# Performance work log

Measured on AMD Instinct MI355X. Metric: run time of the kernel, lower is better.

Reference implementation:

```python
import jax, jax.numpy as jnp
import numpy as np

B, N = 4, 128
INPUT_SIZE, Z_SIZE = 512, 256
D_TENSOR, N_HEADS, SEQ_LEN = 64, 8, 64
D = D_TENSOR * N_HEADS * SEQ_LEN  # 32768


def setup_inputs() -> dict:
    key = jax.random.key(0)
    ks = jax.random.split(key, 10)
    s = lambda fan_in: 1.0 / np.sqrt(fan_in)
    return {
        "x": jax.random.normal(ks[0], (B, N, INPUT_SIZE), dtype=jnp.float32),
        "z": jax.random.normal(ks[1], (B, N, Z_SIZE), dtype=jnp.float32),
        "Wq": jax.random.uniform(ks[2], (Z_SIZE, D), jnp.float32, -s(Z_SIZE), s(Z_SIZE)),
        "bq": jax.random.uniform(ks[3], (D,), jnp.float32, -s(Z_SIZE), s(Z_SIZE)),
        "Wk": jax.random.uniform(ks[4], (INPUT_SIZE, D), jnp.float32, -s(INPUT_SIZE), s(INPUT_SIZE)),
        "bk": jax.random.uniform(ks[5], (D,), jnp.float32, -s(INPUT_SIZE), s(INPUT_SIZE)),
        "Wv": jax.random.uniform(ks[6], (INPUT_SIZE, D), jnp.float32, -s(INPUT_SIZE), s(INPUT_SIZE)),
        "bv": jax.random.uniform(ks[7], (D,), jnp.float32, -s(INPUT_SIZE), s(INPUT_SIZE)),
        "Wo": jax.random.uniform(ks[8], (D, INPUT_SIZE), jnp.float32, -s(D), s(D)),
        "bo": jax.random.uniform(ks[9], (INPUT_SIZE,), jnp.float32, -s(D), s(D)),
    }


def reference(x, z, Wq, bq, Wk, bk, Wv, bv, Wo, bo):
    # Q, K, V: [B, N, heads, seq_len, d_tensor]
    Q = (z @ Wq + bq).reshape(B, N, N_HEADS, SEQ_LEN, D_TENSOR)
    K = (x @ Wk + bk).reshape(B, N, N_HEADS, SEQ_LEN, D_TENSOR)
    V = (x @ Wv + bv).reshape(B, N, N_HEADS, SEQ_LEN, D_TENSOR)
    scores = jnp.einsum("bnhqd,bnhkd->bnhqk", Q, K) / np.sqrt(D_TENSOR).astype(np.float32)
    attn = jax.nn.softmax(scores, axis=-1)
    out = jnp.einsum("bnhqk,bnhkd->bnhqd", attn, V).reshape(B, N, D)
    return out @ Wo + bo
```

## Files before the change

### kernel.cpp

```cpp
#include <hip/hip_runtime.h>
#include <stdint.h>


typedef __attribute__((ext_vector_type(8))) short short8;
typedef __attribute__((ext_vector_type(4))) float floatx4;

__device__ __forceinline__ unsigned short f2bf(float f) {
  union { float f; unsigned int u; } v; v.f = f;
  unsigned int u = v.u + 0x7FFFu + ((v.u >> 16) & 1u);
  return (unsigned short)(u >> 16);
}

#define MFMA16(a, b, c) __builtin_amdgcn_mfma_f32_16x16x32_bf16((a), (b), (c), 0, 0, 0)

#define STAGE_TILE(SRC, LD, LDSARR)                                            \
  do {                                                                         \
    _Pragma("unroll") for (int i_ = 0; i_ < 4; ++i_) {                         \
      int e_ = tid + (i_ << 8);                                                \
      int r_ = e_ >> 3;                                                        \
      int c_ = (e_ & 7) ^ (r_ & 7);                                            \
      __builtin_amdgcn_global_load_lds(                                        \
          (const __attribute__((address_space(1))) unsigned int*)((SRC) +      \
              (size_t)r_ * (LD) + (c_ << 3)),                                  \
          (__attribute__((address_space(3))) unsigned int*)(&(LDSARR)[e_ << 3]),\
          16, 0, 0);                                                           \
    }                                                                          \
  } while (0)

#define FRAG(LDSARR, ROW, KS)                                                  \
  (*(const short8*)(&(LDSARR)[(((ROW) << 6)) +                                 \
      ((((((KS) << 2) + quad)) ^ ((ROW) & 7)) << 3)]))

__device__ __forceinline__ void transpose_body(const float* __restrict__ W,
                                               unsigned short* __restrict__ WT,
                                               int Kd, int Nd) {
  __shared__ __align__(16) float S[64 * 72];
  __shared__ __align__(16) unsigned short T[64 * 72];
  const int tid = threadIdx.x;
  const int n0 = blockIdx.x * 64, k0 = blockIdx.y * 64;
#pragma unroll
  for (int i = 0; i < 4; ++i) {
    int e = tid + (i << 8);
    int r = e >> 4, c = (e & 15) << 2;
    float4 w = *(const float4*)(W + (size_t)(k0 + r) * Nd + n0 + c);
    *(float4*)(&S[r * 72 + c]) = w;
  }
  __syncthreads();
  {
    const int n = tid & 63, kh = tid >> 6;
    float v[16];
#pragma unroll
    for (int j = 0; j < 16; ++j) v[j] = S[(kh * 16 + j) * 72 + n];
    uint4 p0, p1;
    p0.x = f2bf(v[0])  | ((unsigned)f2bf(v[1])  << 16);
    p0.y = f2bf(v[2])  | ((unsigned)f2bf(v[3])  << 16);
    p0.z = f2bf(v[4])  | ((unsigned)f2bf(v[5])  << 16);
    p0.w = f2bf(v[6])  | ((unsigned)f2bf(v[7])  << 16);
    p1.x = f2bf(v[8])  | ((unsigned)f2bf(v[9])  << 16);
    p1.y = f2bf(v[10]) | ((unsigned)f2bf(v[11]) << 16);
    p1.z = f2bf(v[12]) | ((unsigned)f2bf(v[13]) << 16);
    p1.w = f2bf(v[14]) | ((unsigned)f2bf(v[15]) << 16);
    *(uint4*)(&T[n * 72 + kh * 16])     = p0;
    *(uint4*)(&T[n * 72 + kh * 16 + 8]) = p1;
  }
  __syncthreads();
#pragma unroll
  for (int i = 0; i < 2; ++i) {
    int e = tid + (i << 8);
    int n = e >> 3, kc = e & 7;
    uint4 vv = *(const uint4*)(&T[n * 72 + kc * 8]);
    *(uint4*)(WT + (size_t)(n0 + n) * Kd + k0 + kc * 8) = vv;
  }
}

__global__ __launch_bounds__(256) void transpose_qkv(const float* __restrict__ Wq,
                                                     const float* __restrict__ Wk,
                                                     const float* __restrict__ Wv,
                                                     unsigned short* __restrict__ WqT,
                                                     unsigned short* __restrict__ WkT,
                                                     unsigned short* __restrict__ WvT,
                                                     const float* __restrict__ x,
                                                     const float* __restrict__ z,
                                                     unsigned short* __restrict__ xb,
                                                     unsigned short* __restrict__ zb) {
  const int zsel = blockIdx.z;
  if (zsel == 0) {
    if (blockIdx.y >= 4) return;
    transpose_body(Wq, WqT, 256, 32768);
  } else if (zsel == 1) {
    transpose_body(Wk, WkT, 512, 32768);
  } else if (zsel == 2) {
    transpose_body(Wv, WvT, 512, 32768);
  } else {
    if (blockIdx.y != 0 || blockIdx.x >= 192) return;
    int idx = (blockIdx.x * 256 + threadIdx.x) * 8;
    const float* src;
    unsigned short* dst;
    if (idx < 262144) { src = x + idx; dst = xb + idx; }
    else              { src = z + (idx - 262144); dst = zb + (idx - 262144); }
    float4 f0 = *(const float4*)src;
    float4 f1 = *(const float4*)(src + 4);
    uint4 p;
    p.x = f2bf(f0.x) | ((unsigned)f2bf(f0.y) << 16);
    p.y = f2bf(f0.z) | ((unsigned)f2bf(f0.w) << 16);
    p.z = f2bf(f1.x) | ((unsigned)f2bf(f1.y) << 16);
    p.w = f2bf(f1.z) | ((unsigned)f2bf(f1.w) << 16);
    *(uint4*)dst = p;
  }
}

__global__ __launch_bounds__(256) void transpose_wo(const float* __restrict__ W,
                                                    unsigned short* __restrict__ WT) {
  transpose_body(W, WT, 32768, 512);
}

__global__ __launch_bounds__(256) void gemm_qkv(const unsigned short* __restrict__ xb,
                                                const unsigned short* __restrict__ zb,
                                                const unsigned short* __restrict__ WqT,
                                                const unsigned short* __restrict__ WkT,
                                                const unsigned short* __restrict__ WvT,
                                                const float* __restrict__ bq,
                                                const float* __restrict__ bk,
                                                const float* __restrict__ bv,
                                                unsigned short* __restrict__ Qb,
                                                unsigned short* __restrict__ Kb,
                                                unsigned short* __restrict__ Vb) {
  __shared__ __align__(16) unsigned short As[128 * 64];
  __shared__ __align__(16) unsigned short Bs[128 * 64];
  const int tid = threadIdx.x;
  const int zsel = blockIdx.z;
  const unsigned short* A;
  const unsigned short* BT;
  const float* bias;
  unsigned short* C;
  int Ka;
  if (zsel == 0)      { A = zb; BT = WqT; bias = bq; C = Qb; Ka = 256; }
  else if (zsel == 1) { A = xb; BT = WkT; bias = bk; C = Kb; Ka = 512; }
  else                { A = xb; BT = WvT; bias = bv; C = Vb; Ka = 512; }
  const int lane = tid & 63, wid = tid >> 6;
  const int quad = lane >> 4, l15 = lane & 15;
  const int wm = wid >> 1, wn = wid & 1;
  const int m0 = blockIdx.y * 128, n0 = blockIdx.x * 128;
  floatx4 acc[4][4] = {};
  for (int k0 = 0; k0 < Ka; k0 += 64) {
    STAGE_TILE(A + (size_t)m0 * Ka + k0, Ka, As);
    STAGE_TILE(BT + (size_t)n0 * Ka + k0, Ka, Bs);
    __syncthreads();
#pragma unroll
    for (int ks = 0; ks < 2; ++ks) {
      short8 aF[4], bF[4];
#pragma unroll
      for (int mi = 0; mi < 4; ++mi) aF[mi] = FRAG(As, wm * 64 + mi * 16 + l15, ks);
#pragma unroll
      for (int ni = 0; ni < 4; ++ni) bF[ni] = FRAG(Bs, wn * 64 + ni * 16 + l15, ks);
#pragma unroll
      for (int mi = 0; mi < 4; ++mi)
#pragma unroll
        for (int ni = 0; ni < 4; ++ni)
          acc[mi][ni] = MFMA16(aF[mi], bF[ni], acc[mi][ni]);
    }
    __syncthreads();
  }
#pragma unroll
  for (int ni = 0; ni < 4; ++ni) {
    int col = n0 + wn * 64 + ni * 16 + l15;
    float bv2 = bias[col];
#pragma unroll
    for (int mi = 0; mi < 4; ++mi) {
      int row = m0 + wm * 64 + mi * 16 + (quad << 2);
#pragma unroll
      for (int r = 0; r < 4; ++r)
        C[(size_t)(row + r) * 32768 + col] = f2bf(acc[mi][ni][r] + bv2);
    }
  }
}

__global__ __launch_bounds__(256) void attn64(const unsigned short* __restrict__ Qb,
                                              const unsigned short* __restrict__ Kb,
                                              const unsigned short* __restrict__ Vb,
                                              unsigned short* __restrict__ Ob) {
  __shared__ __align__(16) unsigned short Qs[64 * 72];
  __shared__ __align__(16) unsigned short Ks[64 * 72];
  __shared__ __align__(16) unsigned short VT[64 * 72];
  __shared__ __align__(16) unsigned short Ps[64 * 72];
  const int tid = threadIdx.x;
  const int bn = blockIdx.x >> 3, h = blockIdx.x & 7;
  const size_t base = (size_t)bn * 32768 + (size_t)h * 4096;
  const unsigned short* q = Qb + base;
  const unsigned short* k = Kb + base;
  const unsigned short* v = Vb + base;
#pragma unroll
  for (int i = 0; i < 2; ++i) {
    int e = tid + (i << 8);
    int r = e >> 3, dblk = e & 7;
    *(uint4*)(&Qs[r * 72 + dblk * 8]) = *(const uint4*)(q + r * 64 + dblk * 8);
    *(uint4*)(&Ks[r * 72 + dblk * 8]) = *(const uint4*)(k + r * 64 + dblk * 8);
    uint4 vv = *(const uint4*)(v + r * 64 + dblk * 8);
    const unsigned short* pv = (const unsigned short*)&vv;
#pragma unroll
    for (int j = 0; j < 8; ++j)
      VT[(dblk * 8 + j) * 72 + r] = pv[j];
  }
  __syncthreads();
  const int lane = tid & 63, wid = tid >> 6;
  const int quad = lane >> 4, l15 = lane & 15;
  const int qs = wid << 4;
  short8 aq0 = *(const short8*)(&Qs[(qs + l15) * 72 + quad * 8]);
  short8 aq1 = *(const short8*)(&Qs[(qs + l15) * 72 + 32 + quad * 8]);
  floatx4 s[4] = {};
#pragma unroll
  for (int ni = 0; ni < 4; ++ni) {
    short8 b0 = *(const short8*)(&Ks[(ni * 16 + l15) * 72 + quad * 8]);
    short8 b1 = *(const short8*)(&Ks[(ni * 16 + l15) * 72 + 32 + quad * 8]);
    s[ni] = MFMA16(aq0, b0, s[ni]);
    s[ni] = MFMA16(aq1, b1, s[ni]);
  }
#pragma unroll
  for (int r = 0; r < 4; ++r) {
    float e0 = s[0][r] * 0.125f, e1 = s[1][r] * 0.125f;
    float e2 = s[2][r] * 0.125f, e3 = s[3][r] * 0.125f;
    float m = fmaxf(fmaxf(e0, e1), fmaxf(e2, e3));
    m = fmaxf(m, __shfl_xor(m, 1));
    m = fmaxf(m, __shfl_xor(m, 2));
    m = fmaxf(m, __shfl_xor(m, 4));
    m = fmaxf(m, __shfl_xor(m, 8));
    float x0 = __expf(e0 - m), x1 = __expf(e1 - m);
    float x2 = __expf(e2 - m), x3 = __expf(e3 - m);
    float t = x0 + x1 + x2 + x3;
    t += __shfl_xor(t, 1); t += __shfl_xor(t, 2);
    t += __shfl_xor(t, 4); t += __shfl_xor(t, 8);
    float inv = __builtin_amdgcn_rcpf(t);
    int row = qs + (quad << 2) + r;
    Ps[row * 72 +      l15] = f2bf(x0 * inv);
    Ps[row * 72 + 16 + l15] = f2bf(x1 * inv);
    Ps[row * 72 + 32 + l15] = f2bf(x2 * inv);
    Ps[row * 72 + 48 + l15] = f2bf(x3 * inv);
  }
  __syncthreads();
  short8 ap0 = *(const short8*)(&Ps[(qs + l15) * 72 + quad * 8]);
  short8 ap1 = *(const short8*)(&Ps[(qs + l15) * 72 + 32 + quad * 8]);
  floatx4 o[4] = {};
#pragma unroll
  for (int ni = 0; ni < 4; ++ni) {
    short8 b0 = *(const short8*)(&VT[(ni * 16 + l15) * 72 + quad * 8]);
    short8 b1 = *(const short8*)(&VT[(ni * 16 + l15) * 72 + 32 + quad * 8]);
    o[ni] = MFMA16(ap0, b0, o[ni]);
    o[ni] = MFMA16(ap1, b1, o[ni]);
  }
  unsigned short* outp = Ob + base;
#pragma unroll
  for (int ni = 0; ni < 4; ++ni)
#pragma unroll
    for (int r = 0; r < 4; ++r)
      outp[(qs + (quad << 2) + r) * 64 + ni * 16 + l15] = f2bf(o[ni][r]);
}

__global__ __launch_bounds__(256) void gemm_out(const unsigned short* __restrict__ A,
                                                const unsigned short* __restrict__ BT,
                                                const float* __restrict__ bias,
                                                float* __restrict__ C) {
  __shared__ __align__(16) unsigned short As[128 * 64];
  __shared__ __align__(16) unsigned short Bs[128 * 64];
  const int tid = threadIdx.x;
  const int lane = tid & 63, wid = tid >> 6;
  const int quad = lane >> 4, l15 = lane & 15;
  const int wm = wid >> 1, wn = wid & 1;
  const int m0 = blockIdx.y * 128, n0 = blockIdx.x * 128;
  const int kbase = blockIdx.z * 1024;
  floatx4 acc[4][4] = {};
  for (int k0 = kbase; k0 < kbase + 1024; k0 += 64) {
    STAGE_TILE(A + (size_t)m0 * 32768 + k0, 32768, As);
    STAGE_TILE(BT + (size_t)n0 * 32768 + k0, 32768, Bs);
    __syncthreads();
#pragma unroll
    for (int ks = 0; ks < 2; ++ks) {
      short8 aF[4], bF[4];
#pragma unroll
      for (int mi = 0; mi < 4; ++mi) aF[mi] = FRAG(As, wm * 64 + mi * 16 + l15, ks);
#pragma unroll
      for (int ni = 0; ni < 4; ++ni) bF[ni] = FRAG(Bs, wn * 64 + ni * 16 + l15, ks);
#pragma unroll
      for (int mi = 0; mi < 4; ++mi)
#pragma unroll
        for (int ni = 0; ni < 4; ++ni)
          acc[mi][ni] = MFMA16(aF[mi], bF[ni], acc[mi][ni]);
    }
    __syncthreads();
  }
#pragma unroll
  for (int ni = 0; ni < 4; ++ni) {
    int col = n0 + wn * 64 + ni * 16 + l15;
    float bv = (blockIdx.z == 0) ? bias[col] : 0.0f;
#pragma unroll
    for (int mi = 0; mi < 4; ++mi) {
      int row = m0 + wm * 64 + mi * 16 + (quad << 2);
#pragma unroll
      for (int r = 0; r < 4; ++r)
        atomicAdd(&C[(size_t)(row + r) * 512 + col], acc[mi][ni][r] + bv);
    }
  }
}

extern "C" void kernel_launch(void* const* d_in, const int* in_sizes, int n_in,
                              void* d_out, int out_size, void* d_ws, size_t ws_size,
                              hipStream_t stream) {
  const float* x  = (const float*)d_in[0];
  const float* z  = (const float*)d_in[1];
  const float* Wq = (const float*)d_in[2];
  const float* bq = (const float*)d_in[3];
  const float* Wk = (const float*)d_in[4];
  const float* bk = (const float*)d_in[5];
  const float* Wv = (const float*)d_in[6];
  const float* bv = (const float*)d_in[7];
  const float* Wo = (const float*)d_in[8];
  const float* bo = (const float*)d_in[9];
  float* out = (float*)d_out;
  char* ws = (char*)d_ws;

  unsigned short* WqT = (unsigned short*)(ws + 0);
  unsigned short* WkT = (unsigned short*)(ws + 16777216);
  unsigned short* WvT = (unsigned short*)(ws + 50331648);
  unsigned short* Qb  = (unsigned short*)(ws + 83886080);
  unsigned short* Kb  = (unsigned short*)(ws + 117440512);
  unsigned short* Vb  = (unsigned short*)(ws + 150994944);
  unsigned short* Ob  = (unsigned short*)(ws + 0);
  unsigned short* WoT = (unsigned short*)(ws + 50331648);

  unsigned short* xb = (unsigned short*)d_out;
  unsigned short* zb = (unsigned short*)((char*)d_out + 524288);

  transpose_qkv<<<dim3(512, 8, 4), 256, 0, stream>>>(Wq, Wk, Wv, WqT, WkT, WvT,
                                                     x, z, xb, zb);

  gemm_qkv<<<dim3(256, 4, 3), 256, 0, stream>>>(xb, zb, WqT, WkT, WvT,
                                                bq, bk, bv, Qb, Kb, Vb);

  transpose_wo<<<dim3(8, 512), 256, 0, stream>>>(Wo, WoT);

  attn64<<<dim3(4096), 256, 0, stream>>>(Qb, Kb, Vb, Ob);

  hipMemsetAsync(d_out, 0, (size_t)out_size * sizeof(float), stream);
  gemm_out<<<dim3(4, 4, 32), 256, 0, stream>>>(Ob, WoT, bo, out);
}
```

Measured before the change: 384.7 us.

## Fuse fp32 weight conversion into GEMM B-tile staging and drop transpose kernels

```diff
diff --git a/kernel.cpp b/kernel.cpp
--- a/kernel.cpp
+++ b/kernel.cpp
@@ -9,6 +9,12 @@
   union { float f; unsigned int u; } v; v.f = f;
   unsigned int u = v.u + 0x7FFFu + ((v.u >> 16) & 1u);
   return (unsigned short)(u >> 16);
+}
+
+__device__ __forceinline__ unsigned int cvt_pk_bf16(float lo, float hi) {
+  unsigned int r;
+  asm("v_cvt_pk_bf16_f32 %0, %1, %2" : "=v"(r) : "v"(lo), "v"(hi));
+  return r;
 }
 
 #define MFMA16(a, b, c) __builtin_amdgcn_mfma_f32_16x16x32_bf16((a), (b), (c), 0, 0, 0)
@@ -31,120 +37,80 @@
   (*(const short8*)(&(LDSARR)[(((ROW) << 6)) +                                 \
       ((((((KS) << 2) + quad)) ^ ((ROW) & 7)) << 3)]))
 
-__device__ __forceinline__ void transpose_body(const float* __restrict__ W,
-                                               unsigned short* __restrict__ WT,
-                                               int Kd, int Nd) {
-  __shared__ __align__(16) float S[64 * 72];
-  __shared__ __align__(16) unsigned short T[64 * 72];
-  const int tid = threadIdx.x;
-  const int n0 = blockIdx.x * 64, k0 = blockIdx.y * 64;
-#pragma unroll
-  for (int i = 0; i < 4; ++i) {
-    int e = tid + (i << 8);
-    int r = e >> 4, c = (e & 15) << 2;
-    float4 w = *(const float4*)(W + (size_t)(k0 + r) * Nd + n0 + c);
-    *(float4*)(&S[r * 72 + c]) = w;
-  }
-  __syncthreads();
-  {
-    const int n = tid & 63, kh = tid >> 6;
-    float v[16];
-#pragma unroll
-    for (int j = 0; j < 16; ++j) v[j] = S[(kh * 16 + j) * 72 + n];
-    uint4 p0, p1;
-    p0.x = f2bf(v[0])  | ((unsigned)f2bf(v[1])  << 16);
-    p0.y = f2bf(v[2])  | ((unsigned)f2bf(v[3])  << 16);
-    p0.z = f2bf(v[4])  | ((unsigned)f2bf(v[5])  << 16);
-    p0.w = f2bf(v[6])  | ((unsigned)f2bf(v[7])  << 16);
-    p1.x = f2bf(v[8])  | ((unsigned)f2bf(v[9])  << 16);
-    p1.y = f2bf(v[10]) | ((unsigned)f2bf(v[11]) << 16);
-    p1.z = f2bf(v[12]) | ((unsigned)f2bf(v[13]) << 16);
-    p1.w = f2bf(v[14]) | ((unsigned)f2bf(v[15]) << 16);
-    *(uint4*)(&T[n * 72 + kh * 16])     = p0;
-    *(uint4*)(&T[n * 72 + kh * 16 + 8]) = p1;
-  }
-  __syncthreads();
-#pragma unroll
-  for (int i = 0; i < 2; ++i) {
-    int e = tid + (i << 8);
-    int n = e >> 3, kc = e & 7;
-    uint4 vv = *(const uint4*)(&T[n * 72 + kc * 8]);
-    *(uint4*)(WT + (size_t)(n0 + n) * Kd + k0 + kc * 8) = vv;
-  }
-}
-
-__global__ __launch_bounds__(256) void transpose_qkv(const float* __restrict__ Wq,
-                                                     const float* __restrict__ Wk,
-                                                     const float* __restrict__ Wv,
-                                                     unsigned short* __restrict__ WqT,
-                                                     unsigned short* __restrict__ WkT,
-                                                     unsigned short* __restrict__ WvT,
-                                                     const float* __restrict__ x,
-                                                     const float* __restrict__ z,
-                                                     unsigned short* __restrict__ xb,
-                                                     unsigned short* __restrict__ zb) {
-  const int zsel = blockIdx.z;
-  if (zsel == 0) {
-    if (blockIdx.y >= 4) return;
-    transpose_body(Wq, WqT, 256, 32768);
-  } else if (zsel == 1) {
-    transpose_body(Wk, WkT, 512, 32768);
-  } else if (zsel == 2) {
-    transpose_body(Wv, WvT, 512, 32768);
-  } else {
-    if (blockIdx.y != 0 || blockIdx.x >= 192) return;
-    int idx = (blockIdx.x * 256 + threadIdx.x) * 8;
-    const float* src;
-    unsigned short* dst;
-    if (idx < 262144) { src = x + idx; dst = xb + idx; }
-    else              { src = z + (idx - 262144); dst = zb + (idx - 262144); }
-    float4 f0 = *(const float4*)src;
-    float4 f1 = *(const float4*)(src + 4);
+template <int LDW>
+__device__ __forceinline__ void stage_b_f32(const float* __restrict__ Wp,
+                                            unsigned short* Bs, int tid) {
+  const int n = tid & 127;
+  const int octb = __builtin_amdgcn_readfirstlane(tid >> 7);
+#pragma unroll
+  for (int g = 0; g < 4; ++g) {
+    const int oct = octb + 2 * g;
+    const float* src = Wp + (size_t)(oct << 3) * LDW + n;
+    float f[8];
+#pragma unroll
+    for (int j = 0; j < 8; ++j) f[j] = src[(size_t)j * LDW];
     uint4 p;
-    p.x = f2bf(f0.x) | ((unsigned)f2bf(f0.y) << 16);
-    p.y = f2bf(f0.z) | ((unsigned)f2bf(f0.w) << 16);
-    p.z = f2bf(f1.x) | ((unsigned)f2bf(f1.y) << 16);
-    p.w = f2bf(f1.z) | ((unsigned)f2bf(f1.w) << 16);
-    *(uint4*)dst = p;
-  }
-}
-
-__global__ __launch_bounds__(256) void transpose_wo(const float* __restrict__ W,
-                                                    unsigned short* __restrict__ WT) {
-  transpose_body(W, WT, 32768, 512);
-}
-
-__global__ __launch_bounds__(256) void gemm_qkv(const unsigned short* __restrict__ xb,
-                                                const unsigned short* __restrict__ zb,
-                                                const unsigned short* __restrict__ WqT,
-                                                const unsigned short* __restrict__ WkT,
-                                                const unsigned short* __restrict__ WvT,
-                                                const float* __restrict__ bq,
-                                                const float* __restrict__ bk,
-                                                const float* __restrict__ bv,
-                                                unsigned short* __restrict__ Qb,
-                                                unsigned short* __restrict__ Kb,
-                                                unsigned short* __restrict__ Vb) {
+    p.x = cvt_pk_bf16(f[0], f[1]);
+    p.y = cvt_pk_bf16(f[2], f[3]);
+    p.z = cvt_pk_bf16(f[4], f[5]);
+    p.w = cvt_pk_bf16(f[6], f[7]);
+    *(uint4*)(&Bs[(n << 6) + ((oct ^ (n & 7)) << 3)]) = p;
+  }
+}
+
+__global__ __launch_bounds__(256) void convert_xz(const float* __restrict__ x,
+                                                  const float* __restrict__ z,
+                                                  unsigned short* __restrict__ xb,
+                                                  unsigned short* __restrict__ zb) {
+  int idx = (blockIdx.x * 256 + threadIdx.x) * 8;
+  const float* src;
+  unsigned short* dst;
+  if (idx < 262144) { src = x + idx; dst = xb + idx; }
+  else              { src = z + (idx - 262144); dst = zb + (idx - 262144); }
+  float4 f0 = *(const float4*)src;
+  float4 f1 = *(const float4*)(src + 4);
+  uint4 p;
+  p.x = f2bf(f0.x) | ((unsigned)f2bf(f0.y) << 16);
+  p.y = f2bf(f0.z) | ((unsigned)f2bf(f0.w) << 16);
+  p.z = f2bf(f1.x) | ((unsigned)f2bf(f1.y) << 16);
+  p.w = f2bf(f1.z) | ((unsigned)f2bf(f1.w) << 16);
+  *(uint4*)dst = p;
+}
+
+__global__ __launch_bounds__(256, 2) void gemm_qkv(const unsigned short* __restrict__ xb,
+                                                   const unsigned short* __restrict__ zb,
+                                                   const float* __restrict__ Wq,
+                                                   const float* __restrict__ Wk,
+                                                   const float* __restrict__ Wv,
+                                                   const float* __restrict__ bq,
+                                                   const float* __restrict__ bk,
+                                                   const float* __restrict__ bv,
+                                                   unsigned short* __restrict__ Qb,
+                                                   unsigned short* __restrict__ Kb,
+                                                   unsigned short* __restrict__ Vb) {
   __shared__ __align__(16) unsigned short As[128 * 64];
   __shared__ __align__(16) unsigned short Bs[128 * 64];
   const int tid = threadIdx.x;
   const int zsel = blockIdx.z;
   const unsigned short* A;
-  const unsigned short* BT;
+  const float* W;
   const float* bias;
   unsigned short* C;
   int Ka;
-  if (zsel == 0)      { A = zb; BT = WqT; bias = bq; C = Qb; Ka = 256; }
-  else if (zsel == 1) { A = xb; BT = WkT; bias = bk; C = Kb; Ka = 512; }
-  else                { A = xb; BT = WvT; bias = bv; C = Vb; Ka = 512; }
+  if (zsel == 0)      { A = zb; W = Wq; bias = bq; C = Qb; Ka = 256; }
+  else if (zsel == 1) { A = xb; W = Wk; bias = bk; C = Kb; Ka = 512; }
+  else                { A = xb; W = Wv; bias = bv; C = Vb; Ka = 512; }
+  const int id = blockIdx.x;
+  const int xcd = id & 7, bj = id >> 3;
+  const int m0 = (bj & 3) << 7;
+  const int n0 = ((xcd << 5) | (bj >> 2)) << 7;
   const int lane = tid & 63, wid = tid >> 6;
   const int quad = lane >> 4, l15 = lane & 15;
   const int wm = wid >> 1, wn = wid & 1;
-  const int m0 = blockIdx.y * 128, n0 = blockIdx.x * 128;
   floatx4 acc[4][4] = {};
   for (int k0 = 0; k0 < Ka; k0 += 64) {
     STAGE_TILE(A + (size_t)m0 * Ka + k0, Ka, As);
-    STAGE_TILE(BT + (size_t)n0 * Ka + k0, Ka, Bs);
+    stage_b_f32<32768>(W + (size_t)k0 * 32768 + n0, Bs, tid);
     __syncthreads();
 #pragma unroll
     for (int ks = 0; ks < 2; ++ks) {
@@ -255,30 +221,35 @@
       outp[(qs + (quad << 2) + r) * 64 + ni * 16 + l15] = f2bf(o[ni][r]);
 }
 
-__global__ __launch_bounds__(256) void gemm_out(const unsigned short* __restrict__ A,
-                                                const unsigned short* __restrict__ BT,
-                                                const float* __restrict__ bias,
-                                                float* __restrict__ C) {
+__global__ __launch_bounds__(256, 2) void gemm_out(const unsigned short* __restrict__ A,
+                                                   const float* __restrict__ Wo,
+                                                   const float* __restrict__ bias,
+                                                   float* __restrict__ C) {
   __shared__ __align__(16) unsigned short As[128 * 64];
   __shared__ __align__(16) unsigned short Bs[128 * 64];
   const int tid = threadIdx.x;
+  const int id = blockIdx.x;
+  const int xcd = id & 7, bj = id >> 3;
+  const int m0 = (bj & 3) << 7;
+  const int q = bj >> 2;
+  const int n0 = (q & 3) << 7;
+  const int ks = (xcd << 2) | (q >> 2);
+  const int kbase = ks << 10;
   const int lane = tid & 63, wid = tid >> 6;
   const int quad = lane >> 4, l15 = lane & 15;
   const int wm = wid >> 1, wn = wid & 1;
-  const int m0 = blockIdx.y * 128, n0 = blockIdx.x * 128;
-  const int kbase = blockIdx.z * 1024;
   floatx4 acc[4][4] = {};
   for (int k0 = kbase; k0 < kbase + 1024; k0 += 64) {
     STAGE_TILE(A + (size_t)m0 * 32768 + k0, 32768, As);
-    STAGE_TILE(BT + (size_t)n0 * 32768 + k0, 32768, Bs);
+    stage_b_f32<512>(Wo + (size_t)k0 * 512 + n0, Bs, tid);
     __syncthreads();
 #pragma unroll
-    for (int ks = 0; ks < 2; ++ks) {
+    for (int kss = 0; kss < 2; ++kss) {
       short8 aF[4], bF[4];
 #pragma unroll
-      for (int mi = 0; mi < 4; ++mi) aF[mi] = FRAG(As, wm * 64 + mi * 16 + l15, ks);
-#pragma unroll
-      for (int ni = 0; ni < 4; ++ni) bF[ni] = FRAG(Bs, wn * 64 + ni * 16 + l15, ks);
+      for (int mi = 0; mi < 4; ++mi) aF[mi] = FRAG(As, wm * 64 + mi * 16 + l15, kss);
+#pragma unroll
+      for (int ni = 0; ni < 4; ++ni) bF[ni] = FRAG(Bs, wn * 64 + ni * 16 + l15, kss);
 #pragma unroll
       for (int mi = 0; mi < 4; ++mi)
 #pragma unroll
@@ -290,13 +261,13 @@
 #pragma unroll
   for (int ni = 0; ni < 4; ++ni) {
     int col = n0 + wn * 64 + ni * 16 + l15;
-    float bv = (blockIdx.z == 0) ? bias[col] : 0.0f;
+    float bv0 = (ks == 0) ? bias[col] : 0.0f;
 #pragma unroll
     for (int mi = 0; mi < 4; ++mi) {
       int row = m0 + wm * 64 + mi * 16 + (quad << 2);
 #pragma unroll
       for (int r = 0; r < 4; ++r)
-        atomicAdd(&C[(size_t)(row + r) * 512 + col], acc[mi][ni][r] + bv);
+        atomicAdd(&C[(size_t)(row + r) * 512 + col], acc[mi][ni][r] + bv0);
     }
   }
 }
@@ -317,28 +288,20 @@
   float* out = (float*)d_out;
   char* ws = (char*)d_ws;
 
-  unsigned short* WqT = (unsigned short*)(ws + 0);
-  unsigned short* WkT = (unsigned short*)(ws + 16777216);
-  unsigned short* WvT = (unsigned short*)(ws + 50331648);
-  unsigned short* Qb  = (unsigned short*)(ws + 83886080);
-  unsigned short* Kb  = (unsigned short*)(ws + 117440512);
-  unsigned short* Vb  = (unsigned short*)(ws + 150994944);
-  unsigned short* Ob  = (unsigned short*)(ws + 0);
-  unsigned short* WoT = (unsigned short*)(ws + 50331648);
-
-  unsigned short* xb = (unsigned short*)d_out;
-  unsigned short* zb = (unsigned short*)((char*)d_out + 524288);
-
-  transpose_qkv<<<dim3(512, 8, 4), 256, 0, stream>>>(Wq, Wk, Wv, WqT, WkT, WvT,
-                                                     x, z, xb, zb);
-
-  gemm_qkv<<<dim3(256, 4, 3), 256, 0, stream>>>(xb, zb, WqT, WkT, WvT,
-                                                bq, bk, bv, Qb, Kb, Vb);
-
-  transpose_wo<<<dim3(8, 512), 256, 0, stream>>>(Wo, WoT);
+  unsigned short* Qb = (unsigned short*)(ws + 0);
+  unsigned short* Kb = (unsigned short*)(ws + 33554432);
+  unsigned short* Vb = (unsigned short*)(ws + 67108864);
+  unsigned short* Ob = (unsigned short*)(ws + 100663296);
+  unsigned short* xb = (unsigned short*)(ws + 134217728);
+  unsigned short* zb = (unsigned short*)(ws + 134217728 + 524288);
+
+  convert_xz<<<dim3(192), 256, 0, stream>>>(x, z, xb, zb);
+
+  gemm_qkv<<<dim3(1024, 1, 3), 256, 0, stream>>>(xb, zb, Wq, Wk, Wv,
+                                                 bq, bk, bv, Qb, Kb, Vb);
 
   attn64<<<dim3(4096), 256, 0, stream>>>(Qb, Kb, Vb, Ob);
 
   hipMemsetAsync(d_out, 0, (size_t)out_size * sizeof(float), stream);
-  gemm_out<<<dim3(4, 4, 32), 256, 0, stream>>>(Ob, WoT, bo, out);
-}
+  gemm_out<<<dim3(512), 256, 0, stream>>>(Ob, Wo, bo, out);
+}
```

Result: no change. 378.1 us (-1.7%).
